# Optimization experiments

Hardware: AMD Instinct MI355X
Metric: run time of the kernel (lower is better)

The kernel has to match this reference:

```python
import jax, jax.numpy as jnp
import numpy as np
from jax import lax

D_MODEL = 64
D_STATE = 16
D_INNER = 128   # expand * d_model
DT_RANK = 4     # ceil(d_model / 16)
D_CONV = 4      # mamba_ssm default causal conv width
N_MAMBA = 6


def _gelu(x):
    return jax.nn.gelu(x, approximate=False)


def _conv2d(x, w, b, groups=1):
    ph, pw = w.shape[2] // 2, w.shape[3] // 2
    y = lax.conv_general_dilated(x, w, (1, 1), [(ph, ph), (pw, pw)],
                                 dimension_numbers=('NCHW', 'OIHW', 'NCHW'),
                                 feature_group_count=groups)
    return y + b[None, :, None, None]


def _group_norm(x, w, b, groups=4, eps=1e-5):
    B, C, H, W = x.shape
    xr = x.reshape(B, groups, C // groups, H * W)
    m = xr.mean((2, 3), keepdims=True)
    v = ((xr - m) ** 2).mean((2, 3), keepdims=True)
    xr = (xr - m) * lax.rsqrt(v + eps)
    return xr.reshape(B, C, H, W) * w[None, :, None, None] + b[None, :, None, None]


def _res_conv(x, p):
    c1w, c1b, g1w, g1b, c2w, c2b, g2w, g2b = p
    h = _gelu(_group_norm(_conv2d(x, c1w, c1b), g1w, g1b))
    h = _group_norm(_conv2d(h, c2w, c2b), g2w, g2b)
    return _gelu(x + h)


def _mamba(u, in_w, conv_w, conv_b, xproj_w, dt_w, dt_b, A_log, Dp, out_w):
    # u: (B, L, d_model). Standard Mamba-1 selective scan via parallel assoc scan.
    x, z = jnp.split(u @ in_w.T, 2, axis=-1)            # (B,L,Di) each
    # causal depthwise conv1d, kernel D_CONV
    xt = lax.conv_general_dilated(x.transpose(0, 2, 1), conv_w[:, None, :], (1,),
                                  [(D_CONV - 1, 0)],
                                  dimension_numbers=('NCH', 'OIH', 'NCH'),
                                  feature_group_count=D_INNER)
    x = jax.nn.silu((xt + conv_b[None, :, None]).transpose(0, 2, 1))
    dt, Bc, Cc = jnp.split(x @ xproj_w.T, [DT_RANK, DT_RANK + D_STATE], axis=-1)
    dt = jax.nn.softplus(dt @ dt_w.T + dt_b)            # (B,L,Di)
    A = -jnp.exp(A_log)                                  # (Di,N)
    dA = jnp.exp(dt[..., None] * A)                      # (B,L,Di,N)
    dBx = dt[..., None] * Bc[:, :, None, :] * x[..., None]

    def comb(e1, e2):  # h_t = a_t*h_{t-1} + b_t
        a1, b1 = e1
        a2, b2 = e2
        return a1 * a2, b1 * a2 + b2

    _, h = lax.associative_scan(comb, (dA, dBx), axis=1)  # (B,L,Di,N)
    y = jnp.einsum('blds,bls->bld', h, Cc) + Dp * x
    y = y * jax.nn.silu(z)
    return y @ out_w.T


def _bi_mamba(u, mp, i_fwd, i_bwd):
    f = _mamba(u, *[p[i_fwd] for p in mp])
    b = jnp.flip(_mamba(jnp.flip(u, 1), *[p[i_bwd] for p in mp]), 1)
    return 0.5 * (f + b)


def _forward(x, m_in_w, m_conv_w, m_conv_b, m_xproj_w, m_dt_w, m_dt_b, m_A_log,
             m_D, m_out_w, r1_c1_w, r1_c1_b, r1_g1_w, r1_g1_b, r1_c2_w, r1_c2_b,
             r1_g2_w, r1_g2_b, dw_w, dw_b, pw_w, pw_b, r2_c1_w, r2_c1_b, r2_g1_w,
             r2_g1_b, r2_c2_w, r2_c2_b, r2_g2_w, r2_g2_b):
    B, D, H, W = x.shape
    mp = (m_in_w, m_conv_w, m_conv_b, m_xproj_w, m_dt_w, m_dt_b, m_A_log, m_D, m_out_w)
    x_flat = x.reshape(B, D, H * W).transpose(0, 2, 1)   # (B, HW, D)
    # spatial bidirectional mamba
    x_spatial = _bi_mamba(x_flat, mp, 0, 1).transpose(0, 2, 1).reshape(B, D, H, W)
    # local conv branch
    xl = _res_conv(x_spatial, (r1_c1_w, r1_c1_b, r1_g1_w, r1_g1_b, r1_c2_w, r1_c2_b, r1_g2_w, r1_g2_b))
    xl = _gelu(_conv2d(xl, dw_w, dw_b, groups=D))
    xl = _conv2d(xl, pw_w, pw_b)
    xl = _res_conv(xl, (r2_c1_w, r2_c1_b, r2_g1_w, r2_g1_b, r2_c2_w, r2_c2_b, r2_g2_w, r2_g2_b))
    # 'time' branch on original input (same flattening as x_flat)
    x_tg = _bi_mamba(x_flat, mp, 2, 3).transpose(0, 2, 1).reshape(B, D, H, W)
    # downsampled branch
    x_ds = x.reshape(B, D, H // 2, 2, W // 2, 2).mean((3, 5))
    ds_flat = x_ds.reshape(B, D, (H // 2) * (W // 2)).transpose(0, 2, 1)
    x_td = _bi_mamba(ds_flat, mp, 4, 5).transpose(0, 2, 1).reshape(B, D, H // 2, W // 2)
    x_td = jax.image.resize(x_td, (B, D, H, W), method='bilinear')
    return x_spatial + xl + 0.5 * x_tg + 0.5 * x_td


def setup_inputs() -> dict:
    key = jax.random.key(0)
    ks = iter(jax.random.split(key, 64))

    def rn(shape, s=0.02):
        return (s * jax.random.normal(next(ks), shape)).astype(jnp.float32)

    D, Di, N, R = D_MODEL, D_INNER, D_STATE, DT_RANK
    inp = {
        'x': jax.random.normal(next(ks), (2, D, 64, 64), dtype=jnp.float32),
        'm_in_w': rn((N_MAMBA, 2 * Di, D)),
        'm_conv_w': rn((N_MAMBA, Di, D_CONV), 0.1),
        'm_conv_b': rn((N_MAMBA, Di), 0.1),
        'm_xproj_w': rn((N_MAMBA, R + 2 * N, Di)),
        'm_dt_w': rn((N_MAMBA, Di, R), 0.1),
        'm_dt_b': rn((N_MAMBA, Di), 0.5),
        'm_A_log': jnp.tile(jnp.log(jnp.arange(1, N + 1, dtype=jnp.float32)), (N_MAMBA, Di, 1)),
        'm_D': jnp.ones((N_MAMBA, Di), jnp.float32),
        'm_out_w': rn((N_MAMBA, D, Di)),
        'dw_w': rn((D, 1, 3, 3), 0.1), 'dw_b': rn((D,), 0.1),
        'pw_w': rn((D, D, 1, 1), 0.05), 'pw_b': rn((D,), 0.1),
    }
    for pre in ('r1', 'r2'):
        inp[pre + '_c1_w'] = rn((D, D, 3, 3), 0.05)
        inp[pre + '_c1_b'] = rn((D,), 0.1)
        inp[pre + '_g1_w'] = jnp.ones((D,), jnp.float32)
        inp[pre + '_g1_b'] = jnp.zeros((D,), jnp.float32)
        inp[pre + '_c2_w'] = rn((D, D, 3, 3), 0.05)
        inp[pre + '_c2_b'] = rn((D,), 0.1)
        inp[pre + '_g2_w'] = jnp.ones((D,), jnp.float32)
        inp[pre + '_g2_b'] = jnp.zeros((D,), jnp.float32)
    return inp


def reference(x, m_in_w, m_conv_w, m_conv_b, m_xproj_w, m_dt_w, m_dt_b, m_A_log,
              m_D, m_out_w, r1_c1_w, r1_c1_b, r1_g1_w, r1_g1_b, r1_c2_w, r1_c2_b,
              r1_g2_w, r1_g2_b, dw_w, dw_b, pw_w, pw_b, r2_c1_w, r2_c1_b, r2_g1_w,
              r2_g1_b, r2_c2_w, r2_c2_b, r2_g2_w, r2_g2_b):
    return _forward(x, m_in_w, m_conv_w, m_conv_b, m_xproj_w, m_dt_w, m_dt_b,
                    m_A_log, m_D, m_out_w, r1_c1_w, r1_c1_b, r1_g1_w, r1_g1_b,
                    r1_c2_w, r1_c2_b, r1_g2_w, r1_g2_b, dw_w, dw_b, pw_w, pw_b,
                    r2_c1_w, r2_c1_b, r2_g1_w, r2_g1_b, r2_c2_w, r2_c2_b,
                    r2_g2_w, r2_g2_b)
```

## Files before the change

### kernel.cpp

```cpp
#include <hip/hip_runtime.h>
#include <hip/hip_bf16.h>

typedef __hip_bfloat16 bf16;
typedef unsigned short u16;
typedef unsigned int u32;
typedef __attribute__((ext_vector_type(8))) short short8v;
typedef __attribute__((ext_vector_type(4))) float f32x4;


#define XCB_OFF   0u
#define DTB_OFF   2359296u
#define BCB_OFF   4718592u
#define CHA_OFF   5308416u
#define CHH_OFF   7667712u
#define XZ_OFF    10027008u
#define UFS_OFF   14745600u
#define UFD_OFF   15269888u
#define XS_OFF    15400960u
#define XTG_OFF   15925248u
#define XTD_OFF   16449536u
#define XSB_OFF   16580608u
#define WT4_OFF   16842752u
#define STATS_OFF 16916480u
#define FLAG_OFF  16916736u
#define PRM_OFF   16916752u
#define CV0_OFF   0u
#define CV1_OFF   524288u
#define A1B_OFF   1048576u
#define A2B_OFF   1310720u
#define PWB_OFF   1572864u

__device__ __forceinline__ float bits2f(u16 v){
  u32 u = ((u32)v) << 16; float f; __builtin_memcpy(&f, &u, 4); return f;
}
__device__ __forceinline__ float b2f(bf16 v){ return __bfloat162float(v); }
__device__ __forceinline__ u16 f2bu(float f){ bf16 h = __float2bfloat16(f); u16 b; __builtin_memcpy(&b, &h, 2); return b; }
__device__ __forceinline__ float silu_f(float x){ return x / (1.f + __expf(-x)); }
__device__ __forceinline__ float softplus_f(float x){ return fmaxf(x, 0.f) + log1pf(__expf(-fabsf(x))); }
__device__ __forceinline__ float gelu_f(float x){ return 0.5f * x * (1.f + erff(x * 0.70710678118654752f)); }
__device__ __forceinline__ short8v zero8(){ short8v z = {0,0,0,0,0,0,0,0}; return z; }
__device__ __forceinline__ void up2(u32 w, float& a, float& b){
  a = bits2f((u16)(w & 0xffffu)); b = bits2f((u16)(w >> 16));
}
__device__ __forceinline__ void powchain(float r, float* aa){
  aa[0]=r; aa[1]=r*r; aa[2]=aa[1]*r; aa[3]=aa[1]*aa[1];
  aa[4]=aa[3]*r; aa[5]=aa[3]*aa[1]; aa[6]=aa[3]*aa[2]; aa[7]=aa[3]*aa[3];
  aa[8]=aa[7]*r; aa[9]=aa[7]*aa[1]; aa[10]=aa[7]*aa[2]; aa[11]=aa[7]*aa[3];
  aa[12]=aa[7]*aa[4]; aa[13]=aa[7]*aa[5]; aa[14]=aa[7]*aa[6]; aa[15]=aa[7]*aa[7];
}

struct P29 { const void* p[29]; };

__constant__ int PREF[30] = {0, 98304, 101376, 102144, 129792, 132864, 133632,
  145920, 146688, 195840, 196416, 196480, 200576, 200640, 237504, 237568,
  237632, 237696, 274560, 274624, 274688, 274752, 311616, 311680, 311744,
  311808, 348672, 348736, 348800, 348864};

__constant__ float LOGT[16] = {0.0f, 0.6931472f, 1.0986123f, 1.3862944f,
  1.6094379f, 1.7917595f, 1.9459101f, 2.0794415f, 2.1972246f, 2.3025851f,
  2.3978953f, 2.4849067f, 2.5649493f, 2.6390573f, 2.7080502f, 2.7725887f};

__global__ void k_detect(const void* __restrict__ xraw, const void* __restrict__ araw,
                         float* __restrict__ ws){
  __shared__ int cnt_s, bad_s;
  int tid = threadIdx.x;
  if (tid == 0){ cnt_s = 0; bad_s = 0; }
  __syncthreads();
  const u16* p = (const u16*)xraw;
  int c = 0;
  for (int i = tid; i < 4096; i += 256){
    int e = (p[i] >> 7) & 0xFF;
    if (e >= 0x77 && e <= 0x87) c++;
  }
  atomicAdd(&cnt_s, c);
  __syncthreads();
  int flag = (cnt_s > 3500) ? 0 : 1;
  int bad = 0;
  for (int i = tid; i < 12288; i += 256){
    float v = flag ? ((const float*)araw)[i] : b2f(((const bf16*)araw)[i]);
    if (fabsf(v - LOGT[i & 15]) > 0.02f) bad = 1;
  }
  if (bad) atomicAdd(&bad_s, 1);
  __syncthreads();
  if (tid == 0){
    ((int*)(ws + FLAG_OFF))[0] = flag;
    ((int*)(ws + FLAG_OFF))[1] = (bad_s == 0) ? 1 : 0;
  }
}

__global__ __launch_bounds__(256) void k_cvt(P29 ptrs, float* __restrict__ ws){
  int i = blockIdx.x * 256 + threadIdx.x;
  if (i >= 348864) return;
  int flag = *(const int*)(ws + FLAG_OFF);
  int t = 0;
  #pragma unroll 1
  while (i >= PREF[t + 1]) ++t;
  int off = i - PREF[t];
  float v = flag ? ((const float*)ptrs.p[t])[off]
                 : b2f(((const bf16*)ptrs.p[t])[off]);
  ((bf16*)(ws + PRM_OFF))[i] = __float2bfloat16(v);
}

__global__ __launch_bounds__(256) void k_wprep(const bf16* __restrict__ prm_b, bf16* __restrict__ wt4){
  int i = blockIdx.x * 256 + threadIdx.x;
  if (i >= 147456) return;
  int conv = i / 36864, r = i - conv * 36864;
  int tap = r >> 12, co = (r >> 6) & 63, ci = r & 63;
  const int CWOFF[4] = {200640, 237696, 274752, 311808};
  wt4[i] = prm_b[CWOFF[conv] + co * 576 + ci * 9 + tap];
}

__global__ void k_prep(const void* __restrict__ xraw, float* __restrict__ ws){
  int flag = *(const int*)(ws + FLAG_OFF);
  const float* xf = (const float*)xraw;
  const bf16*  xb = (const bf16*)xraw;
  int i = blockIdx.x * 256 + threadIdx.x;
  if (i < 524288){
    int b = i >> 18, rem = i & 262143, l = rem >> 6, d = rem & 63;
    size_t idx = (size_t)b*262144 + d*4096 + l;
    ws[UFS_OFF + i] = flag ? xf[idx] : b2f(xb[idx]);
  } else if (i < 655360){
    int j = i - 524288;
    int b = j >> 16, rem = j & 65535, l = rem >> 6, d = rem & 63;
    int i2 = l >> 5, j2 = l & 31;
    size_t base = (size_t)b*262144 + d*4096 + (i2*2)*64 + j2*2;
    float v0, v1, v2, v3;
    if (flag){ v0 = xf[base]; v1 = xf[base+1]; v2 = xf[base+64]; v3 = xf[base+65]; }
    else     { v0 = b2f(xb[base]); v1 = b2f(xb[base+1]); v2 = b2f(xb[base+64]); v3 = b2f(xb[base+65]); }
    ws[UFD_OFF + j] = 0.25f * (v0 + v1 + v2 + v3);
  }
}

__device__ __forceinline__ void chunk_map(int bid, int& g, int& c0){
  if (bid < 1024){ g = bid >> 7; c0 = bid & 127; }
  else { int r = bid - 1024; g = 8 + (r >> 5); c0 = r & 31; }
}

__global__ __launch_bounds__(256) void k_inproj(const float* __restrict__ ws,
        bf16* __restrict__ XZ, const bf16* __restrict__ in_w){
  __shared__ __align__(16) u16 u_s[32][72];
  int g, tile; chunk_map(blockIdx.x, g, tile);
  int dir = (g < 8) ? (g >> 1) : 4 + ((g - 8) >> 1);
  int b   = (g < 8) ? (g & 1) : ((g - 8) & 1);
  int rev = dir & 1;
  int L   = (g < 8) ? 4096 : 1024;
  int row0 = (g < 8) ? g * 4096 : 32768 + (g - 8) * 1024;
  int t0 = tile * 32;
  const float* U = (g < 8) ? (ws + UFS_OFF + (size_t)b * 262144)
                           : (ws + UFD_OFF + (size_t)b * 65536);
  int tid = threadIdx.x;
  for (int e = tid; e < 2048; e += 256){
    int i = e >> 6, d = e & 63;
    int l = rev ? (L - 1 - (t0 + i)) : (t0 + i);
    u_s[i][d] = f2bu(U[(size_t)l * 64 + d]);
  }
  __syncthreads();
  int w = tid >> 6, lane = tid & 63;
  int l15 = lane & 15, ko = lane >> 4;
  short8v Au[2][2];
  #pragma unroll
  for (int mt = 0; mt < 2; ++mt)
    #pragma unroll
    for (int kk = 0; kk < 2; ++kk)
      Au[mt][kk] = *(const short8v*)&u_s[mt * 16 + l15][kk * 32 + ko * 8];
  const u16* wg = (const u16*)in_w + (size_t)dir * 16384;
  u16* XZu = (u16*)XZ;
  #pragma unroll
  for (int nq = 0; nq < 4; ++nq){
    int nt = w * 4 + nq;
    int c = nt * 16 + l15;
    short8v B0 = *(const short8v*)(wg + (size_t)c * 64 + ko * 8);
    short8v B1 = *(const short8v*)(wg + (size_t)c * 64 + 32 + ko * 8);
    #pragma unroll
    for (int mt = 0; mt < 2; ++mt){
      f32x4 acc = {0.f, 0.f, 0.f, 0.f};
      acc = __builtin_amdgcn_mfma_f32_16x16x32_bf16(Au[mt][0], B0, acc, 0, 0, 0);
      acc = __builtin_amdgcn_mfma_f32_16x16x32_bf16(Au[mt][1], B1, acc, 0, 0, 0);
      #pragma unroll
      for (int reg = 0; reg < 4; ++reg){
        int t = t0 + mt * 16 + ko * 4 + reg;
        XZu[(size_t)(row0 + t) * 256 + c] = f2bu(acc[reg]);
      }
    }
  }
}

__global__ __launch_bounds__(256) void k_front(float* __restrict__ ws,
        const bf16* __restrict__ xproj_w, const bf16* __restrict__ dt_w, const bf16* __restrict__ dt_b,
        const bf16* __restrict__ conv_w, const bf16* __restrict__ conv_b, const bf16* __restrict__ A_log){
  __shared__ __align__(16) u32 xstage[2310];
  __shared__ __align__(16) u16 xc_s[32][136];
  __shared__ __align__(16) u32 blob[4352];
  float* xp_s = (float*)xstage;
  u16* xw_s = (u16*)blob;
  float* cmb = (float*)blob;

  int g, c0; chunk_map(blockIdx.x, g, c0);
  int dir = (g < 8) ? (g >> 1) : 4 + ((g - 8) >> 1);
  int grow0 = (g < 8) ? g * 4096 : 32768 + (g - 8) * 1024;
  int t0 = c0 << 5;
  int crow = ((g < 8) ? g * 128 : 1024 + (g - 8) * 32) + c0;
  int tid = threadIdx.x;

  const u32* XZ32 = (const u32*)(ws + XZ_OFF);
  for (int e = tid; e < 2240; e += 256){
    int lr = e >> 6, col = e & 63;
    int gt = t0 - 3 + lr;
    u32 v = 0u;
    if (gt >= 0) v = XZ32[(size_t)(grow0 + gt) * 128 + col];
    xstage[lr * 66 + col] = v;
  }
  const u16* xw = (const u16*)xproj_w + (size_t)dir * 4608;
  for (int e = tid; e < 6144; e += 256){
    int m = e >> 7, col = e & 127;
    xw_s[m * 136 + col] = (m < 36) ? xw[m * 128 + col] : (u16)0;
  }
  __syncthreads();

  int c = tid & 127, hf = tid >> 7;
  int rb = hf * 16;
  {
    const u16* cwp = (const u16*)conv_w + (size_t)dir * 512 + c * 4;
    uint2 cw2 = *(const uint2*)cwp;
    float cw0, cw1, cw2f, cw3;
    up2(cw2.x, cw0, cw1); up2(cw2.y, cw2f, cw3);
    float cb = b2f(conv_b[dir * 128 + c]);
    const u16* xsu = (const u16*)xstage;
    float xm3 = bits2f(xsu[rb * 132 + c]);
    float xm2 = bits2f(xsu[(rb + 1) * 132 + c]);
    float xm1 = bits2f(xsu[(rb + 2) * 132 + c]);
    u16* XCBu = (u16*)(ws + XCB_OFF);
    #pragma unroll 4
    for (int t = 0; t < 16; ++t){
      float xcur = bits2f(xsu[(rb + t + 3) * 132 + c]);
      float s = cb + cw0 * xm3 + cw1 * xm2 + cw2f * xm1 + cw3 * xcur;
      u16 xbv = f2bu(silu_f(s));
      xm3 = xm2; xm2 = xm1; xm1 = xcur;
      xc_s[rb + t][c] = xbv;
      XCBu[(size_t)(grow0 + t0 + rb + t) * 128 + c] = xbv;
    }
  }
  __syncthreads();

  {
    int w = tid >> 6, lane = tid & 63;
    int l15 = lane & 15, ko = lane >> 4;
    for (int task = w; task < 6; task += 4){
      int mt = task & 1, nt = task >> 1;
      f32x4 acc = {0.f, 0.f, 0.f, 0.f};
      #pragma unroll
      for (int kk = 0; kk < 4; ++kk){
        short8v Afr = *(const short8v*)&xc_s[mt * 16 + l15][kk * 32 + ko * 8];
        short8v Bfr = *(const short8v*)(xw_s + (size_t)(nt * 16 + l15) * 136 + kk * 32 + ko * 8);
        acc = __builtin_amdgcn_mfma_f32_16x16x32_bf16(Afr, Bfr, acc, 0, 0, 0);
      }
      int j = nt * 16 + l15;
      if (j < 36){
        #pragma unroll
        for (int reg = 0; reg < 4; ++reg){
          int t = mt * 16 + ko * 4 + reg;
          xp_s[t * 40 + j] = acc[reg];
        }
      }
    }
  }
  __syncthreads();

  {
    u16* BCBu = (u16*)(ws + BCB_OFF);
    for (int e = tid; e < 1024; e += 256){
      int t = e >> 5, v = e & 31;
      float val = xp_s[t * 40 + 4 + v];
      u16 r = f2bu(val);
      xp_s[t * 40 + 4 + v] = bits2f(r);
      BCBu[(size_t)(grow0 + t0 + t) * 32 + v] = r;
    }
  }
  __syncthreads();

  {
    int apat = ((const int*)(ws + FLAG_OFF))[1];
    float A[16];
    const u16* ap = (const u16*)A_log + (size_t)dir * 2048 + c * 16;
    #pragma unroll
    for (int s = 0; s < 16; ++s) A[s] = -__expf(bits2f(ap[s]));
    const u16* dwp = (const u16*)dt_w + (size_t)dir * 512 + c * 4;
    uint2 dw2 = *(const uint2*)dwp;
    float d0, d1, d2, d3;
    up2(dw2.x, d0, d1); up2(dw2.y, d2, d3);
    float db = b2f(dt_b[dir * 128 + c]);
    u16* DTBu = (u16*)(ws + DTB_OFF);
    float hh[16], p[16];
    #pragma unroll
    for (int s = 0; s < 16; ++s){ hh[s] = 0.f; p[s] = 1.f; }
    float dtsum = 0.f;
    #pragma unroll 2
    for (int t = 0; t < 16; ++t){
      float4 xp4 = *(const float4*)&xp_s[(rb + t) * 40];
      float dtv = softplus_f(db + d0 * xp4.x + d1 * xp4.y + d2 * xp4.z + d3 * xp4.w);
      u16 dtb16 = f2bu(dtv);
      DTBu[(size_t)(grow0 + t0 + rb + t) * 128 + c] = dtb16;
      float dtu = bits2f(dtb16);
      float xcv = bits2f(xc_s[rb + t][c]);
      float dx = dtu * xcv;
      float aa[16];
      if (apat){
        dtsum += dtu;
        powchain(__expf(-dtu), aa);
      } else {
        #pragma unroll
        for (int s = 0; s < 16; ++s) aa[s] = __expf(dtu * A[s]);
        #pragma unroll
        for (int s = 0; s < 16; ++s) p[s] *= aa[s];
      }
      #pragma unroll
      for (int s = 0; s < 16; ++s)
        hh[s] = fmaf(aa[s], hh[s], dx * xp_s[(rb + t) * 40 + 4 + s]);
    }
    if (apat) powchain(__expf(-dtsum), p);
    if (hf == 0){
      #pragma unroll
      for (int s = 0; s < 16; ++s){
        cmb[c * 17 + s] = p[s];
        cmb[2176 + c * 17 + s] = hh[s];
      }
    }
    __syncthreads();
    if (hf == 1){
      float ca[16], ch[16];
      #pragma unroll
      for (int s = 0; s < 16; ++s){
        float P0 = cmb[c * 17 + s];
        float H0 = cmb[2176 + c * 17 + s];
        ca[s] = P0 * p[s];
        ch[s] = fmaf(p[s], H0, hh[s]);
      }
      float* CA = ws + CHA_OFF + (size_t)crow * 2048 + c * 16;
      float* CH = ws + CHH_OFF + (size_t)crow * 2048 + c * 16;
      #pragma unroll
      for (int q = 0; q < 4; ++q){
        *(float4*)(CA + q * 4) = make_float4(ca[q*4], ca[q*4+1], ca[q*4+2], ca[q*4+3]);
        *(float4*)(CH + q * 4) = make_float4(ch[q*4], ch[q*4+1], ch[q*4+2], ch[q*4+3]);
      }
    }
  }
}

__global__ __launch_bounds__(256) void k_scan2(float* __restrict__ ws){
  int id = blockIdx.x * 256 + threadIdx.x;
  int gi = id >> 11, dsl = id & 2047;
  int nc = (gi < 8) ? 128 : 32;
  int cb = (gi < 8) ? gi * 128 : 1024 + (gi - 8) * 32;
  float* CA = ws + CHA_OFF; float* CH = ws + CHH_OFF;
  float hprev = 0.f;
  for (int ch = 0; ch < nc; ch += 8){
    size_t i0 = (size_t)(cb + ch) * 2048 + dsl;
    float a[8], hv[8];
    #pragma unroll
    for (int j = 0; j < 8; ++j){
      a[j] = CA[i0 + (size_t)j * 2048];
      hv[j] = CH[i0 + (size_t)j * 2048];
    }
    #pragma unroll
    for (int j = 0; j < 8; ++j){
      CH[i0 + (size_t)j * 2048] = hprev;
      hprev = fmaf(a[j], hprev, hv[j]);
    }
  }
}

__global__ __launch_bounds__(128) void k_scan3(float* __restrict__ ws, const bf16* __restrict__ A_log,
                                               const bf16* __restrict__ Dp){
  int g, c0; chunk_map(blockIdx.x, g, c0);
  int dir = (g < 8) ? (g >> 1) : 4 + ((g - 8) >> 1);
  int row0 = ((g < 8) ? g * 4096 : 32768 + (g - 8) * 1024) + (c0 << 5);
  int crow = ((g < 8) ? g * 128 : 1024 + (g - 8) * 32) + c0;
  int d = threadIdx.x;
  int apat = ((const int*)(ws + FLAG_OFF))[1];
  float A[16];
  const u16* ap = (const u16*)A_log + (size_t)dir * 2048 + d * 16;
  #pragma unroll
  for (int s = 0; s < 16; ++s) A[s] = -__expf(bits2f(ap[s]));
  float h[16];
  const float* CH = ws + CHH_OFF + (size_t)crow * 2048 + d * 16;
  #pragma unroll
  for (int s = 0; s < 16; ++s) h[s] = CH[s];
  float Dv = b2f(Dp[dir * 128 + d]);
  u16* XCBu = (u16*)(ws + XCB_OFF);
  const u16* DTBu = (const u16*)(ws + DTB_OFF);
  const u16* BCBu = (const u16*)(ws + BCB_OFF);
  const u16* XZu  = (const u16*)(ws + XZ_OFF);
  #pragma unroll 2
  for (int t = 0; t < 32; ++t){
    size_t r = (size_t)(row0 + t);
    float dtu = bits2f(DTBu[r * 128 + d]);
    float xcv = bits2f(XCBu[r * 128 + d]);
    float zv  = bits2f(XZu[r * 256 + 128 + d]);
    const uint4* bp = (const uint4*)(BCBu + r * 32);
    uint4 q0 = bp[0], q1 = bp[1], q2 = bp[2], q3 = bp[3];
    float Bv[16], Cv[16];
    up2(q0.x, Bv[0], Bv[1]);  up2(q0.y, Bv[2], Bv[3]);  up2(q0.z, Bv[4], Bv[5]);  up2(q0.w, Bv[6], Bv[7]);
    up2(q1.x, Bv[8], Bv[9]);  up2(q1.y, Bv[10], Bv[11]); up2(q1.z, Bv[12], Bv[13]); up2(q1.w, Bv[14], Bv[15]);
    up2(q2.x, Cv[0], Cv[1]);  up2(q2.y, Cv[2], Cv[3]);  up2(q2.z, Cv[4], Cv[5]);  up2(q2.w, Cv[6], Cv[7]);
    up2(q3.x, Cv[8], Cv[9]);  up2(q3.y, Cv[10], Cv[11]); up2(q3.z, Cv[12], Cv[13]); up2(q3.w, Cv[14], Cv[15]);
    float dx = dtu * xcv;
    float aa[16];
    if (apat){
      powchain(__expf(-dtu), aa);
    } else {
      #pragma unroll
      for (int s = 0; s < 16; ++s) aa[s] = __expf(dtu * A[s]);
    }
    float y = 0.f;
    #pragma unroll
    for (int s = 0; s < 16; ++s){
      h[s] = fmaf(aa[s], h[s], dx * Bv[s]);
      y = fmaf(h[s], Cv[s], y);
    }
    y = fmaf(Dv, xcv, y);
    XCBu[r * 128 + d] = f2bu(y * silu_f(zv));
  }
}

__global__ __launch_bounds__(256) void k_outproj(float* __restrict__ ws, const bf16* __restrict__ out_w){
  __shared__ __align__(16) u16 yf_s[32][132];
  __shared__ __align__(16) u16 yb_s[32][132];
  int bid = blockIdx.x;
  int pair, b, tile, L;
  if (bid < 512){ pair = bid >> 8; b = (bid >> 7) & 1; tile = bid & 127; L = 4096; }
  else { int r = bid - 512; pair = 2; b = r >> 5; tile = r & 31; L = 1024; }
  int l0 = tile * 32;
  int df = pair * 2, db_ = df + 1;
  int gf = (pair < 2) ? df * 2 + b : 8 + b;
  int gb = (pair < 2) ? db_ * 2 + b : 10 + b;
  int rowf0 = (gf < 8) ? gf * 4096 : 32768 + (gf - 8) * 1024;
  int rowb0 = (gb < 8) ? gb * 4096 : 32768 + (gb - 8) * 1024;
  const u32* Y32 = (const u32*)(ws + XCB_OFF);
  int tid = threadIdx.x;
  for (int e = tid; e < 2048; e += 256){
    int t = e >> 6, kd = e & 63;
    ((u32*)&yf_s[t][0])[kd] = Y32[(size_t)(rowf0 + l0 + t) * 64 + kd];
    ((u32*)&yb_s[t][0])[kd] = Y32[(size_t)(rowb0 + (L - 1 - l0 - t)) * 64 + kd];
  }
  __syncthreads();
  int w = tid >> 6, lane = tid & 63;
  int l15 = lane & 15, ko = lane >> 4;
  int mt = w & 1, nh = w >> 1;
  const u16* wf = (const u16*)out_w + (size_t)df * 8192;
  const u16* wb = (const u16*)out_w + (size_t)db_ * 8192;
  short8v Af[4], Ab[4];
  #pragma unroll
  for (int kk = 0; kk < 4; ++kk){
    Af[kk] = *(const short8v*)&yf_s[mt * 16 + l15][kk * 32 + ko * 8];
    Ab[kk] = *(const short8v*)&yb_s[mt * 16 + l15][kk * 32 + ko * 8];
  }
  float* xo = ws + ((pair == 0) ? XS_OFF : (pair == 1) ? XTG_OFF : XTD_OFF);
  int Lout = (pair < 2) ? 4096 : 1024;
  u16* xsb = (u16*)(ws + XSB_OFF);
  #pragma unroll
  for (int ct = 0; ct < 2; ++ct){
    int c = nh * 32 + ct * 16 + l15;
    f32x4 acc = {0.f, 0.f, 0.f, 0.f};
    #pragma unroll
    for (int kk = 0; kk < 4; ++kk){
      short8v Bf = *(const short8v*)(wf + (size_t)c * 128 + kk * 32 + ko * 8);
      acc = __builtin_amdgcn_mfma_f32_16x16x32_bf16(Af[kk], Bf, acc, 0, 0, 0);
      short8v Bb = *(const short8v*)(wb + (size_t)c * 128 + kk * 32 + ko * 8);
      acc = __builtin_amdgcn_mfma_f32_16x16x32_bf16(Ab[kk], Bb, acc, 0, 0, 0);
    }
    #pragma unroll
    for (int reg = 0; reg < 4; ++reg){
      int row = l0 + mt * 16 + ko * 4 + reg;
      float v = 0.5f * acc[reg];
      xo[((size_t)b * Lout + row) * 64 + c] = v;
      if (pair == 0) xsb[((size_t)b * 4096 + row) * 64 + c] = f2bu(v);
    }
  }
}

template<int NTAP>
__global__ __launch_bounds__(256) void k_convmfma(const bf16* __restrict__ act,
        float* __restrict__ outf, bf16* __restrict__ outb,
        const bf16* __restrict__ wt, const bf16* __restrict__ bias){
  int wid = blockIdx.x * 4 + (threadIdx.x >> 6);
  int lane = threadIdx.x & 63;
  int nc = wid & 1;
  int pt = wid >> 1;
  int b = pt >> 8, py = (pt >> 2) & 63, x0 = (pt & 3) << 4;
  int l15 = lane & 15, ko = lane >> 4;
  f32x4 acc0 = {0.f, 0.f, 0.f, 0.f}, acc1 = {0.f, 0.f, 0.f, 0.f};
  const bf16* ab = act + ((size_t)b * 4096) * 64;
  #pragma unroll
  for (int tap = 0; tap < NTAP; ++tap){
    int dy = (NTAP == 9) ? (tap / 3 - 1) : 0;
    int dx = (NTAP == 9) ? (tap % 3 - 1) : 0;
    int y = py + dy;
    if (NTAP == 9){ if ((unsigned)y >= 64u) continue; }
    int xx = x0 + l15 + dx;
    bool vall = (NTAP == 1) || ((unsigned)xx < 64u);
    const bf16* arow = ab + ((size_t)(y * 64 + xx)) * 64;
    const bf16* wrow = wt + (size_t)tap * 4096;
    #pragma unroll
    for (int kk = 0; kk < 2; ++kk){
      int ci0 = kk * 32 + ko * 8;
      short8v a;
      if (vall) a = *(const short8v*)(arow + ci0); else a = zero8();
      short8v bw0 = *(const short8v*)(wrow + (size_t)(nc * 32 + l15) * 64 + ci0);
      short8v bw1 = *(const short8v*)(wrow + (size_t)(nc * 32 + 16 + l15) * 64 + ci0);
      acc0 = __builtin_amdgcn_mfma_f32_16x16x32_bf16(a, bw0, acc0, 0, 0, 0);
      acc1 = __builtin_amdgcn_mfma_f32_16x16x32_bf16(a, bw1, acc1, 0, 0, 0);
    }
  }
  float bs0 = b2f(bias[nc * 32 + l15]);
  float bs1 = b2f(bias[nc * 32 + 16 + l15]);
  size_t obase = ((size_t)b * 4096 + py * 64 + x0 + (ko << 2)) * 64 + nc * 32;
  if (outf){
    #pragma unroll
    for (int r = 0; r < 4; ++r){
      outf[obase + (size_t)r * 64 + l15] = acc0[r] + bs0;
      outf[obase + (size_t)r * 64 + 16 + l15] = acc1[r] + bs1;
    }
  } else {
    #pragma unroll
    for (int r = 0; r < 4; ++r){
      outb[obase + (size_t)r * 64 + l15] = __float2bfloat16(acc0[r] + bs0);
      outb[obase + (size_t)r * 64 + 16 + l15] = __float2bfloat16(acc1[r] + bs1);
    }
  }
}

__global__ __launch_bounds__(256) void k_statsP(const float* __restrict__ in, float* __restrict__ out){
  __shared__ float red[8];
  int bid = blockIdx.x;
  int bg = bid >> 2, qq = bid & 3;
  int b = bg >> 2, g = bg & 3;
  int tid = threadIdx.x;
  float s1 = 0.f, s2 = 0.f;
  for (int e = tid; e < 4096; e += 256){
    int px = qq * 1024 + (e >> 2), q4 = e & 3;
    float4 v = *(const float4*)(in + ((size_t)b * 4096 + px) * 64 + g * 16 + q4 * 4);
    s1 += v.x + v.y + v.z + v.w;
    s2 += v.x*v.x + v.y*v.y + v.z*v.z + v.w*v.w;
  }
  #pragma unroll
  for (int off = 32; off; off >>= 1){ s1 += __shfl_down(s1, off, 64); s2 += __shfl_down(s2, off, 64); }
  int wid = tid >> 6;
  if ((tid & 63) == 0){ red[wid] = s1; red[wid + 4] = s2; }
  __syncthreads();
  if (tid == 0){
    out[bg * 8 + qq * 2] = red[0] + red[1] + red[2] + red[3];
    out[bg * 8 + qq * 2 + 1] = red[4] + red[5] + red[6] + red[7];
  }
}

__global__ __launch_bounds__(256) void k_gn_act(const float* __restrict__ in, const float* __restrict__ res,
        bf16* __restrict__ outb, const float* __restrict__ st,
        const bf16* __restrict__ gw, const bf16* __restrict__ gb, int add_res){
  int t = blockIdx.x * 256 + threadIdx.x;
  int cq = t & 15, px = (t >> 4) & 4095, b = t >> 16;
  int c0 = cq * 4, g = cq >> 2;
  const float* sp = st + (b * 4 + g) * 8;
  float s1 = sp[0] + sp[2] + sp[4] + sp[6];
  float s2 = sp[1] + sp[3] + sp[5] + sp[7];
  float mean = s1 * (1.f / 65536.f);
  float rs = rsqrtf(s2 * (1.f / 65536.f) - mean * mean + 1e-5f);
  size_t idx = ((size_t)b * 4096 + px) * 64 + c0;
  float4 f = *(const float4*)(in + idx);
  float vv[4] = {f.x, f.y, f.z, f.w};
  float rr[4] = {0.f, 0.f, 0.f, 0.f};
  if (add_res){ float4 r4 = *(const float4*)(res + idx); rr[0]=r4.x; rr[1]=r4.y; rr[2]=r4.z; rr[3]=r4.w; }
  u16 o[4];
  #pragma unroll
  for (int j = 0; j < 4; ++j){
    float v = (vv[j] - mean) * rs * b2f(gw[c0 + j]) + b2f(gb[c0 + j]);
    v += rr[j];
    o[j] = f2bu(gelu_f(v));
  }
  u32 lo = (u32)o[0] | ((u32)o[1] << 16);
  u32 hi = (u32)o[2] | ((u32)o[3] << 16);
  *(uint2*)((u16*)outb + idx) = make_uint2(lo, hi);
}

__global__ __launch_bounds__(256) void k_dwgelu(const bf16* __restrict__ in, bf16* __restrict__ out,
        const bf16* __restrict__ w, const bf16* __restrict__ bias){
  int id = blockIdx.x * 256 + threadIdx.x;
  int oc8 = id & 7, px = (id >> 3) & 4095, b = id >> 15;
  int py = px >> 6, pxx = px & 63;
  float wv[8][9];
  #pragma unroll
  for (int j = 0; j < 8; ++j)
    #pragma unroll
    for (int tp = 0; tp < 9; ++tp) wv[j][tp] = b2f(w[(oc8 * 8 + j) * 9 + tp]);
  float acc[8];
  #pragma unroll
  for (int j = 0; j < 8; ++j) acc[j] = b2f(bias[oc8 * 8 + j]);
  const bf16* inb = in + ((size_t)b * 4096) * 64;
  #pragma unroll
  for (int dy = 0; dy < 3; ++dy){
    int y = py + dy - 1;
    if ((unsigned)y >= 64u) continue;
    #pragma unroll
    for (int dx = 0; dx < 3; ++dx){
      int x = pxx + dx - 1;
      if ((unsigned)x >= 64u) continue;
      short8v iv = *(const short8v*)(inb + ((size_t)(y * 64 + x)) * 64 + oc8 * 8);
      #pragma unroll
      for (int j = 0; j < 8; ++j)
        acc[j] = fmaf(bits2f((u16)iv[j]), wv[j][dy * 3 + dx], acc[j]);
    }
  }
  u32 pk[4];
  #pragma unroll
  for (int k = 0; k < 4; ++k){
    u16 a0 = f2bu(gelu_f(acc[2 * k]));
    u16 a1 = f2bu(gelu_f(acc[2 * k + 1]));
    pk[k] = (u32)a0 | ((u32)a1 << 16);
  }
  *(uint4*)((u16*)out + ((size_t)b * 4096 + px) * 64 + oc8 * 8) = make_uint4(pk[0], pk[1], pk[2], pk[3]);
}

__global__ __launch_bounds__(256) void k_final(const float* __restrict__ ws, void* __restrict__ outp,
        const bf16* __restrict__ gw, const bf16* __restrict__ gb){
  int flag = *(const int*)(ws + FLAG_OFF);
  int bid = blockIdx.x;
  int b = bid >> 6, py = bid & 63;
  int t = threadIdx.x;
  int c = t & 63, pxg = t >> 6;
  int g = c >> 4;
  const float* sp = ws + STATS_OFF + 3 * 64 + (b * 4 + g) * 8;
  float s1 = sp[0] + sp[2] + sp[4] + sp[6];
  float s2 = sp[1] + sp[3] + sp[5] + sp[7];
  float mean = s1 * (1.f / 65536.f);
  float rs = rsqrtf(s2 * (1.f / 65536.f) - mean * mean + 1e-5f);
  float gwv = b2f(gw[c]), gbv = b2f(gb[c]);
  const float* CV1 = ws + CV1_OFF;
  const bf16* PWB = (const bf16*)(ws + PWB_OFF);
  const float* XS = ws + XS_OFF;
  const float* XTG = ws + XTG_OFF;
  const float* XTD = ws + XTD_OFF + ((size_t)b * 1024) * 64;
  float sy = 0.5f * py - 0.25f;
  float fly = floorf(sy); float fy = sy - fly;
  int iy0 = max((int)fly, 0), iy1 = min((int)fly + 1, 31);
  float of[16];
  #pragma unroll
  for (int i = 0; i < 16; ++i){
    int px = pxg * 16 + i;
    size_t idx = ((size_t)b * 4096 + py * 64 + px) * 64 + c;
    float gn = (CV1[idx] - mean) * rs * gwv + gbv;
    float xl = gelu_f(b2f(PWB[idx]) + gn);
    float sx = 0.5f * px - 0.25f;
    float flx = floorf(sx); float fx = sx - flx;
    int ix0 = max((int)flx, 0), ix1 = min((int)flx + 1, 31);
    float v00 = XTD[(size_t)(iy0 * 32 + ix0) * 64 + c], v01 = XTD[(size_t)(iy0 * 32 + ix1) * 64 + c];
    float v10 = XTD[(size_t)(iy1 * 32 + ix0) * 64 + c], v11 = XTD[(size_t)(iy1 * 32 + ix1) * 64 + c];
    float tdv = (1.f - fy) * ((1.f - fx) * v00 + fx * v01) + fy * ((1.f - fx) * v10 + fx * v11);
    of[i] = XS[idx] + xl + 0.5f * XTG[idx] + 0.5f * tdv;
  }
  size_t ob = ((size_t)(b * 64 + c)) * 4096 + py * 64 + pxg * 16;
  if (flag){
    float* o = (float*)outp + ob;
    #pragma unroll
    for (int k = 0; k < 4; ++k)
      *(float4*)(o + k * 4) = make_float4(of[k*4], of[k*4+1], of[k*4+2], of[k*4+3]);
  } else {
    u16* o = (u16*)outp + ob;
    u32 pk[8];
    #pragma unroll
    for (int k = 0; k < 8; ++k)
      pk[k] = (u32)f2bu(of[2*k]) | ((u32)f2bu(of[2*k+1]) << 16);
    *(uint4*)(o) = make_uint4(pk[0], pk[1], pk[2], pk[3]);
    *(uint4*)(o + 8) = make_uint4(pk[4], pk[5], pk[6], pk[7]);
  }
}

extern "C" void kernel_launch(void* const* d_in, const int* in_sizes, int n_in,
                              void* d_out, int out_size, void* d_ws, size_t ws_size,
                              hipStream_t stream) {
  float* ws = (float*)d_ws;
  bf16* XZ = (bf16*)(ws + XZ_OFF);
  bf16* prm = (bf16*)(ws + PRM_OFF);
  bf16* WT4 = (bf16*)(ws + WT4_OFF);
  bf16* XSB = (bf16*)(ws + XSB_OFF);
  bf16* A1B = (bf16*)(ws + A1B_OFF);
  bf16* A2B = (bf16*)(ws + A2B_OFF);
  bf16* PWBb = (bf16*)(ws + PWB_OFF);
  float* CV0 = ws + CV0_OFF;
  float* CV1 = ws + CV1_OFF;
  float* ST = ws + STATS_OFF;

  const bf16* m_in_w   = prm + 0;
  const bf16* m_conv_w = prm + 98304;
  const bf16* m_conv_b = prm + 101376;
  const bf16* m_xproj  = prm + 102144;
  const bf16* m_dt_w   = prm + 129792;
  const bf16* m_dt_b   = prm + 132864;
  const bf16* m_A_log  = prm + 133632;
  const bf16* m_D      = prm + 145920;
  const bf16* m_out_w  = prm + 146688;
  const bf16* dw_w  = prm + 195840;
  const bf16* dw_b  = prm + 196416;
  const bf16* pw_w  = prm + 196480;
  const bf16* pw_b  = prm + 200576;
  const bf16* r1c1b = prm + 237504;
  const bf16* r1g1w = prm + 237568;
  const bf16* r1g1b = prm + 237632;
  const bf16* r1c2b = prm + 274560;
  const bf16* r1g2w = prm + 274624;
  const bf16* r1g2b = prm + 274688;
  const bf16* r2c1b = prm + 311616;
  const bf16* r2g1w = prm + 311680;
  const bf16* r2g1b = prm + 311744;
  const bf16* r2c2b = prm + 348672;
  const bf16* r2g2w = prm + 348736;
  const bf16* r2g2b = prm + 348800;

  P29 ptrs;
  for (int t = 0; t < 29; ++t) ptrs.p[t] = d_in[t + 1];

  k_detect<<<1, 256, 0, stream>>>(d_in[0], d_in[7], ws);
  k_cvt<<<1363, 256, 0, stream>>>(ptrs, ws);
  k_prep<<<2560, 256, 0, stream>>>(d_in[0], ws);
  k_wprep<<<576, 256, 0, stream>>>(prm, WT4);
  k_inproj<<<1152, 256, 0, stream>>>(ws, XZ, m_in_w);
  k_front<<<1152, 256, 0, stream>>>(ws, m_xproj, m_dt_w, m_dt_b, m_conv_w, m_conv_b, m_A_log);
  k_scan2<<<96, 256, 0, stream>>>(ws);
  k_scan3<<<1152, 128, 0, stream>>>(ws, m_A_log, m_D);
  k_outproj<<<576, 256, 0, stream>>>(ws, m_out_w);

  k_convmfma<9><<<256, 256, 0, stream>>>(XSB, CV0, (bf16*)nullptr, WT4 + 0 * 36864, r1c1b);
  k_statsP<<<32, 256, 0, stream>>>(CV0, ST + 0 * 64);
  k_gn_act<<<512, 256, 0, stream>>>(CV0, (const float*)nullptr, A1B, ST + 0 * 64, r1g1w, r1g1b, 0);
  k_convmfma<9><<<256, 256, 0, stream>>>(A1B, CV1, (bf16*)nullptr, WT4 + 1 * 36864, r1c2b);
  k_statsP<<<32, 256, 0, stream>>>(CV1, ST + 1 * 64);
  k_gn_act<<<512, 256, 0, stream>>>(CV1, ws + XS_OFF, A2B, ST + 1 * 64, r1g2w, r1g2b, 1);
  k_dwgelu<<<256, 256, 0, stream>>>(A2B, A1B, dw_w, dw_b);
  k_convmfma<1><<<256, 256, 0, stream>>>(A1B, (float*)nullptr, PWBb, pw_w, pw_b);
  k_convmfma<9><<<256, 256, 0, stream>>>(PWBb, CV0, (bf16*)nullptr, WT4 + 2 * 36864, r2c1b);
  k_statsP<<<32, 256, 0, stream>>>(CV0, ST + 2 * 64);
  k_gn_act<<<512, 256, 0, stream>>>(CV0, (const float*)nullptr, A1B, ST + 2 * 64, r2g1w, r2g1b, 0);
  k_convmfma<9><<<256, 256, 0, stream>>>(A1B, CV1, (bf16*)nullptr, WT4 + 3 * 36864, r2c2b);
  k_statsP<<<32, 256, 0, stream>>>(CV1, ST + 3 * 64);
  k_final<<<128, 256, 0, stream>>>(ws, d_out, r2g2w, r2g2b);
}
```

Baseline: 246.7 us.

## Fuse chunk scan output pass into out-projection kernel via shared memory

The final selective-scan pass (per-chunk state propagation producing gated y) is moved into the out-projection kernel. Each 256-thread block runs the 32-step scan for a forward chunk and the matching reversed backward chunk, writing bf16 y directly into shared memory tiles. This removes one launch and the global write-back and reload of y. In exchange the out-projection blocks now carry the serial scan latency, and the extra registers may lower occupancy.

```diff
diff --git a/kernel.cpp b/kernel.cpp
--- a/kernel.cpp
+++ b/kernel.cpp
@@ -369,60 +369,8 @@
   }
 }
 
-__global__ __launch_bounds__(128) void k_scan3(float* __restrict__ ws, const bf16* __restrict__ A_log,
-                                               const bf16* __restrict__ Dp){
-  int g, c0; chunk_map(blockIdx.x, g, c0);
-  int dir = (g < 8) ? (g >> 1) : 4 + ((g - 8) >> 1);
-  int row0 = ((g < 8) ? g * 4096 : 32768 + (g - 8) * 1024) + (c0 << 5);
-  int crow = ((g < 8) ? g * 128 : 1024 + (g - 8) * 32) + c0;
-  int d = threadIdx.x;
-  int apat = ((const int*)(ws + FLAG_OFF))[1];
-  float A[16];
-  const u16* ap = (const u16*)A_log + (size_t)dir * 2048 + d * 16;
-  #pragma unroll
-  for (int s = 0; s < 16; ++s) A[s] = -__expf(bits2f(ap[s]));
-  float h[16];
-  const float* CH = ws + CHH_OFF + (size_t)crow * 2048 + d * 16;
-  #pragma unroll
-  for (int s = 0; s < 16; ++s) h[s] = CH[s];
-  float Dv = b2f(Dp[dir * 128 + d]);
-  u16* XCBu = (u16*)(ws + XCB_OFF);
-  const u16* DTBu = (const u16*)(ws + DTB_OFF);
-  const u16* BCBu = (const u16*)(ws + BCB_OFF);
-  const u16* XZu  = (const u16*)(ws + XZ_OFF);
-  #pragma unroll 2
-  for (int t = 0; t < 32; ++t){
-    size_t r = (size_t)(row0 + t);
-    float dtu = bits2f(DTBu[r * 128 + d]);
-    float xcv = bits2f(XCBu[r * 128 + d]);
-    float zv  = bits2f(XZu[r * 256 + 128 + d]);
-    const uint4* bp = (const uint4*)(BCBu + r * 32);
-    uint4 q0 = bp[0], q1 = bp[1], q2 = bp[2], q3 = bp[3];
-    float Bv[16], Cv[16];
-    up2(q0.x, Bv[0], Bv[1]);  up2(q0.y, Bv[2], Bv[3]);  up2(q0.z, Bv[4], Bv[5]);  up2(q0.w, Bv[6], Bv[7]);
-    up2(q1.x, Bv[8], Bv[9]);  up2(q1.y, Bv[10], Bv[11]); up2(q1.z, Bv[12], Bv[13]); up2(q1.w, Bv[14], Bv[15]);
-    up2(q2.x, Cv[0], Cv[1]);  up2(q2.y, Cv[2], Cv[3]);  up2(q2.z, Cv[4], Cv[5]);  up2(q2.w, Cv[6], Cv[7]);
-    up2(q3.x, Cv[8], Cv[9]);  up2(q3.y, Cv[10], Cv[11]); up2(q3.z, Cv[12], Cv[13]); up2(q3.w, Cv[14], Cv[15]);
-    float dx = dtu * xcv;
-    float aa[16];
-    if (apat){
-      powchain(__expf(-dtu), aa);
-    } else {
-      #pragma unroll
-      for (int s = 0; s < 16; ++s) aa[s] = __expf(dtu * A[s]);
-    }
-    float y = 0.f;
-    #pragma unroll
-    for (int s = 0; s < 16; ++s){
-      h[s] = fmaf(aa[s], h[s], dx * Bv[s]);
-      y = fmaf(h[s], Cv[s], y);
-    }
-    y = fmaf(Dv, xcv, y);
-    XCBu[r * 128 + d] = f2bu(y * silu_f(zv));
-  }
-}
-
-__global__ __launch_bounds__(256) void k_outproj(float* __restrict__ ws, const bf16* __restrict__ out_w){
+__global__ __launch_bounds__(256) void k_outproj(float* __restrict__ ws, const bf16* __restrict__ out_w,
+        const bf16* __restrict__ A_log, const bf16* __restrict__ Dp){
   __shared__ __align__(16) u16 yf_s[32][132];
   __shared__ __align__(16) u16 yb_s[32][132];
   int bid = blockIdx.x;
@@ -430,19 +378,70 @@
   if (bid < 512){ pair = bid >> 8; b = (bid >> 7) & 1; tile = bid & 127; L = 4096; }
   else { int r = bid - 512; pair = 2; b = r >> 5; tile = r & 31; L = 1024; }
   int l0 = tile * 32;
+  int ncht = L >> 5;
   int df = pair * 2, db_ = df + 1;
   int gf = (pair < 2) ? df * 2 + b : 8 + b;
   int gb = (pair < 2) ? db_ * 2 + b : 10 + b;
   int rowf0 = (gf < 8) ? gf * 4096 : 32768 + (gf - 8) * 1024;
   int rowb0 = (gb < 8) ? gb * 4096 : 32768 + (gb - 8) * 1024;
-  const u32* Y32 = (const u32*)(ws + XCB_OFF);
   int tid = threadIdx.x;
-  for (int e = tid; e < 2048; e += 256){
-    int t = e >> 6, kd = e & 63;
-    ((u32*)&yf_s[t][0])[kd] = Y32[(size_t)(rowf0 + l0 + t) * 64 + kd];
-    ((u32*)&yb_s[t][0])[kd] = Y32[(size_t)(rowb0 + (L - 1 - l0 - t)) * 64 + kd];
-  }
-  __syncthreads();
+
+  {
+    int half = tid >> 7, d = tid & 127;
+    int gS = half ? gb : gf;
+    int dirS = (gS < 8) ? (gS >> 1) : 4 + ((gS - 8) >> 1);
+    int rowS = half ? (rowb0 + (L - 32 - l0)) : (rowf0 + l0);
+    int cbaseS = (gS < 8) ? gS * 128 : 1024 + (gS - 8) * 32;
+    int crowS = cbaseS + (half ? (ncht - 1 - tile) : tile);
+    int apat = ((const int*)(ws + FLAG_OFF))[1];
+    float A[16];
+    const u16* ap = (const u16*)A_log + (size_t)dirS * 2048 + d * 16;
+    #pragma unroll
+    for (int s = 0; s < 16; ++s) A[s] = -__expf(bits2f(ap[s]));
+    float h[16];
+    const float* CH = ws + CHH_OFF + (size_t)crowS * 2048 + d * 16;
+    #pragma unroll
+    for (int s = 0; s < 16; ++s) h[s] = CH[s];
+    float Dv = b2f(Dp[dirS * 128 + d]);
+    const u16* XCBu = (const u16*)(ws + XCB_OFF);
+    const u16* DTBu = (const u16*)(ws + DTB_OFF);
+    const u16* BCBu = (const u16*)(ws + BCB_OFF);
+    const u16* XZu  = (const u16*)(ws + XZ_OFF);
+    #pragma unroll 2
+    for (int t = 0; t < 32; ++t){
+      size_t r = (size_t)(rowS + t);
+      float dtu = bits2f(DTBu[r * 128 + d]);
+      float xcv = bits2f(XCBu[r * 128 + d]);
+      float zv  = bits2f(XZu[r * 256 + 128 + d]);
+      const uint4* bp = (const uint4*)(BCBu + r * 32);
+      uint4 q0 = bp[0], q1 = bp[1], q2 = bp[2], q3 = bp[3];
+      float Bv[16], Cv[16];
+      up2(q0.x, Bv[0], Bv[1]);  up2(q0.y, Bv[2], Bv[3]);  up2(q0.z, Bv[4], Bv[5]);  up2(q0.w, Bv[6], Bv[7]);
+      up2(q1.x, Bv[8], Bv[9]);  up2(q1.y, Bv[10], Bv[11]); up2(q1.z, Bv[12], Bv[13]); up2(q1.w, Bv[14], Bv[15]);
+      up2(q2.x, Cv[0], Cv[1]);  up2(q2.y, Cv[2], Cv[3]);  up2(q2.z, Cv[4], Cv[5]);  up2(q2.w, Cv[6], Cv[7]);
+      up2(q3.x, Cv[8], Cv[9]);  up2(q3.y, Cv[10], Cv[11]); up2(q3.z, Cv[12], Cv[13]); up2(q3.w, Cv[14], Cv[15]);
+      float dx = dtu * xcv;
+      float aa[16];
+      if (apat){
+        powchain(__expf(-dtu), aa);
+      } else {
+        #pragma unroll
+        for (int s = 0; s < 16; ++s) aa[s] = __expf(dtu * A[s]);
+      }
+      float y = 0.f;
+      #pragma unroll
+      for (int s = 0; s < 16; ++s){
+        h[s] = fmaf(aa[s], h[s], dx * Bv[s]);
+        y = fmaf(h[s], Cv[s], y);
+      }
+      y = fmaf(Dv, xcv, y);
+      u16 yv = f2bu(y * silu_f(zv));
+      if (half == 0) yf_s[t][d] = yv;
+      else           yb_s[31 - t][d] = yv;
+    }
+  }
+  __syncthreads();
+
   int w = tid >> 6, lane = tid & 63;
   int l15 = lane & 15, ko = lane >> 4;
   int mt = w & 1, nh = w >> 1;
@@ -724,8 +723,7 @@
   k_inproj<<<1152, 256, 0, stream>>>(ws, XZ, m_in_w);
   k_front<<<1152, 256, 0, stream>>>(ws, m_xproj, m_dt_w, m_dt_b, m_conv_w, m_conv_b, m_A_log);
   k_scan2<<<96, 256, 0, stream>>>(ws);
-  k_scan3<<<1152, 128, 0, stream>>>(ws, m_A_log, m_D);
-  k_outproj<<<576, 256, 0, stream>>>(ws, m_out_w);
+  k_outproj<<<576, 256, 0, stream>>>(ws, m_out_w, m_A_log, m_D);
 
   k_convmfma<9><<<256, 256, 0, stream>>>(XSB, CV0, (bf16*)nullptr, WT4 + 0 * 36864, r1c1b);
   k_statsP<<<32, 256, 0, stream>>>(CV0, ST + 0 * 64);
```

After: 238.4 us. 3.4% less time.
